# Performance work log

Measured on AMD Instinct MI355X. Metric: run time of the kernel, lower is better.

## Reference

```python
import jax, jax.numpy as jnp
import numpy as np

DIM = 1024
LN_EPS = 1e-5


def setup_inputs() -> dict:
    key = jax.random.key(0)
    ks = jax.random.split(key, 6)
    B, S, D = 8, 2048, DIM
    x = jax.random.normal(ks[0], (B, S, D), dtype=jnp.float32)
    mask = jnp.ones((B, S, 1), dtype=jnp.float32)
    # LayerNorm params
    ln_g = jnp.ones((D,), dtype=jnp.float32)
    ln_b = jnp.zeros((D,), dtype=jnp.float32)
    # FeedForward: Linear(D, D) -> GELU -> Linear(D, D); hidden_dim == dim per source
    lim = 1.0 / np.sqrt(D)
    w1 = jax.random.uniform(ks[1], (D, D), jnp.float32, -lim, lim)
    b1 = jax.random.uniform(ks[2], (D,), jnp.float32, -lim, lim)
    w2 = jax.random.uniform(ks[3], (D, D), jnp.float32, -lim, lim)
    b2 = jax.random.uniform(ks[4], (D,), jnp.float32, -lim, lim)
    return {"x": x, "mask": mask, "ln_g": ln_g, "ln_b": ln_b,
            "w1": w1, "b1": b1, "w2": w2, "b2": b2}


def _layernorm(t, g, b):
    mu = jnp.mean(t, axis=-1, keepdims=True)
    var = jnp.mean(jnp.square(t - mu), axis=-1, keepdims=True)
    return (t - mu) * jax.lax.rsqrt(var + LN_EPS) * g + b


def reference(x, mask, ln_g, ln_b, w1, b1, w2, b2):
    # torch.fft(t, signal_ndim=1): FFT over hidden axis (complex input, imag=0)
    ft = jnp.fft.fft(x.astype(jnp.float32), axis=-1)
    # torch.fft(., signal_ndim=2): 2D FFT over (seq, hidden)
    ft = jnp.fft.fft2(ft, axes=(-2, -1))
    ft = ft.real  # [..., 0] slice of the fake-complex tensor
    t = _layernorm(x + ft, ln_g, ln_b)
    # FeedForward: Linear -> GELU(exact) -> Linear (dropout is identity at eval)
    h = jax.nn.gelu(t @ w1 + b1, approximate=False)
    out = h @ w2 + b2
    return out * mask
```

## Files before the change

kernel.cpp:

```cpp
#include <hip/hip_runtime.h>
#include <math.h>

#define DIMD 1024
#define SEQ  2048
#define BATCH 8
#define ROWS (BATCH * SEQ)

#define MF 1152
#define KF 1088

typedef __attribute__((ext_vector_type(8))) short bf16x8;
typedef __attribute__((ext_vector_type(4))) float f32x4;
typedef __attribute__((ext_vector_type(8))) unsigned short ushort8;

__device__ __forceinline__ unsigned short f2bf(float f) {
    unsigned u = __float_as_uint(f);
    unsigned r = (u + 0x7FFFu + ((u >> 16) & 1u)) >> 16;
    return (unsigned short)r;
}
__device__ __forceinline__ float bf2f(unsigned short h) {
    return __uint_as_float(((unsigned)h) << 16);
}
__device__ __forceinline__ void gl_lds16(const void* g, void* l) {
    __builtin_amdgcn_global_load_lds(
        (const __attribute__((address_space(1))) unsigned int*)g,
        (__attribute__((address_space(3))) unsigned int*)l, 16, 0, 0);
}


__global__ __launch_bounds__(256) void build_acos(unsigned short* __restrict__ Acos) {
    int s = blockIdx.x;
    for (int t = threadIdx.x; t < KF; t += 256) {
        float c = 0.0f;
        if (t <= 1024) {
            int prod = (s * t) & (SEQ - 1);
            c = cospif((float)prod * (1.0f / 1024.0f));
        }
        Acos[(size_t)s * KF + t] = f2bf(c);
    }
}

__global__ __launch_bounds__(256) void build_xe(const float* __restrict__ x,
                                                unsigned short* __restrict__ Xe) {
    int lane = threadIdx.x & 63;
    int oct  = threadIdx.x >> 6;
    int n = blockIdx.x * 64 + lane;
    int b = n >> 10, d = n & 1023;
    int rd = (DIMD - d) & (DIMD - 1);
    int t0 = blockIdx.y * 32 + oct * 8;
    const float* xb = x + (size_t)b * SEQ * DIMD + rd;
    ushort8 tmp;
    #pragma unroll
    for (int j = 0; j < 8; ++j) {
        int t = t0 + j;
        float v;
        if (t == 0)          v = xb[0];
        else if (t < 1024)   v = xb[(size_t)t * DIMD] + xb[(size_t)(2048 - t) * DIMD];
        else if (t == 1024)  v = xb[(size_t)1024 * DIMD];
        else                 v = 0.0f;
        tmp[j] = f2bf(v);
    }
    *(ushort8*)&Xe[(size_t)n * KF + t0] = tmp;
}

__global__ __launch_bounds__(256) void pack_wt(const float* __restrict__ W,
                                               unsigned short* __restrict__ Wt) {
    int lane = threadIdx.x & 63;
    int oct = threadIdx.x >> 6;
    int n = blockIdx.x * 64 + lane;
    int k0 = blockIdx.y * 32 + oct * 8;
    ushort8 tmp;
    #pragma unroll
    for (int j = 0; j < 8; ++j) tmp[j] = f2bf(W[(size_t)(k0 + j) * DIMD + n]);
    *(ushort8*)&Wt[(size_t)n * DIMD + k0] = tmp;
}

template <int MODE>
__global__ __launch_bounds__(256) void gemm_bt(const unsigned short* __restrict__ A,
                                               const unsigned short* __restrict__ B,
                                               int K, int lda, int ldb, int ldc,
                                               const float* __restrict__ xres,
                                               const float* __restrict__ bias,
                                               const float* __restrict__ mask,
                                               void* __restrict__ outp) {
    __shared__ unsigned short As[128 * 64];
    __shared__ unsigned short Bs[128 * 64];

    const int tid = threadIdx.x;
    const int lane = tid & 63;
    const int wv = tid >> 6;
    const int wm = wv & 1;
    const int wn = wv >> 1;
    const int fr = lane & 15;
    const int quad = lane >> 4;

    int bx = blockIdx.x, by = blockIdx.y;
    if (MODE != 0) {
        int lin = bx + 8 * by;
        int c = lin & 7;
        int g = lin >> 3;
        bx = g & 7;
        by = (g >> 3) * 8 + c;
    }
    const int m0 = by * 128;
    const int n0 = bx * 128;

    const int st_row = (lane >> 3);
    const int st_col = (lane & 7) * 8;

    f32x4 acc[4][4] = {};

    for (int k0 = 0; k0 < K; k0 += 64) {
        __syncthreads();
        #pragma unroll
        for (int i = 0; i < 4; ++i) {
            int chunk = wv * 4 + i;
            int ar = m0 + chunk * 8 + st_row;
            int br = n0 + chunk * 8 + st_row;
            gl_lds16(&A[(size_t)ar * lda + k0 + st_col], &As[chunk * 512]);
            gl_lds16(&B[(size_t)br * ldb + k0 + st_col], &Bs[chunk * 512]);
        }
        __syncthreads();

        #pragma unroll
        for (int ks = 0; ks < 2; ++ks) {
            bf16x8 af[4], bfv[4];
            #pragma unroll
            for (int i = 0; i < 4; ++i)
                af[i] = *(const bf16x8*)&As[(wm * 64 + i * 16 + fr) * 64 + ks * 32 + quad * 8];
            #pragma unroll
            for (int j = 0; j < 4; ++j)
                bfv[j] = *(const bf16x8*)&Bs[(wn * 64 + j * 16 + fr) * 64 + ks * 32 + quad * 8];
            #pragma unroll
            for (int i = 0; i < 4; ++i)
                #pragma unroll
                for (int j = 0; j < 4; ++j)
                    acc[i][j] = __builtin_amdgcn_mfma_f32_16x16x32_bf16(af[i], bfv[j], acc[i][j], 0, 0, 0);
        }
    }

    #pragma unroll
    for (int i = 0; i < 4; ++i) {
        int rowb = m0 + wm * 64 + i * 16 + quad * 4;
        #pragma unroll
        for (int j = 0; j < 4; ++j) {
            int col = n0 + wn * 64 + j * 16 + fr;
            #pragma unroll
            for (int r = 0; r < 4; ++r) {
                float v = acc[i][j][r];
                int row = rowb + r;
                if (MODE == 0) {
                    int s = row;
                    if (s <= 1024) {
                        int b = col >> 10, d = col & 1023;
                        unsigned short* y = (unsigned short*)outp;
                        size_t i1 = ((size_t)b * SEQ + s) * DIMD + d;
                        y[i1] = f2bf(xres[i1] + 1024.0f * v);
                        if (s >= 1 && s <= 1023) {
                            size_t i2 = ((size_t)b * SEQ + (2048 - s)) * DIMD + d;
                            y[i2] = f2bf(xres[i2] + 1024.0f * v);
                        }
                    }
                } else if (MODE == 1) {
                    v += bias[col];
                    v = 0.5f * v * (1.0f + erff(v * 0.70710678118654752f));
                    ((unsigned short*)outp)[(size_t)row * ldc + col] = f2bf(v);
                } else {
                    v += bias[col];
                    v *= mask[row];
                    ((float*)outp)[(size_t)row * ldc + col] = v;
                }
            }
        }
    }
}

__global__ __launch_bounds__(256) void ln_bf(const unsigned short* __restrict__ y,
                                             const float* __restrict__ g,
                                             const float* __restrict__ beta,
                                             unsigned short* __restrict__ t) {
    const int row = blockIdx.x;
    ushort4 raw = ((const ushort4*)(y + (size_t)row * DIMD))[threadIdx.x];
    float v0 = bf2f(raw.x), v1 = bf2f(raw.y), v2 = bf2f(raw.z), v3 = bf2f(raw.w);

    __shared__ float red[4];
    const int wave = threadIdx.x >> 6;
    const int lane = threadIdx.x & 63;

    float sm = v0 + v1 + v2 + v3;
    #pragma unroll
    for (int off = 32; off > 0; off >>= 1) sm += __shfl_down(sm, off, 64);
    if (lane == 0) red[wave] = sm;
    __syncthreads();
    const float mean = (red[0] + red[1] + red[2] + red[3]) * (1.0f / DIMD);

    float dx0 = v0 - mean, dx1 = v1 - mean, dx2 = v2 - mean, dx3 = v3 - mean;
    float q = dx0 * dx0 + dx1 * dx1 + dx2 * dx2 + dx3 * dx3;
    __syncthreads();
    #pragma unroll
    for (int off = 32; off > 0; off >>= 1) q += __shfl_down(q, off, 64);
    if (lane == 0) red[wave] = q;
    __syncthreads();
    const float var = (red[0] + red[1] + red[2] + red[3]) * (1.0f / DIMD);
    const float rstd = rsqrtf(var + 1e-5f);

    float4 g4 = ((const float4*)g)[threadIdx.x];
    float4 b4 = ((const float4*)beta)[threadIdx.x];
    ushort4 o;
    o.x = f2bf(dx0 * rstd * g4.x + b4.x);
    o.y = f2bf(dx1 * rstd * g4.y + b4.y);
    o.z = f2bf(dx2 * rstd * g4.z + b4.z);
    o.w = f2bf(dx3 * rstd * g4.w + b4.w);
    ((ushort4*)(t + (size_t)row * DIMD))[threadIdx.x] = o;
}

#define BM 64
#define BN 64
#define BK 16

__global__ __launch_bounds__(256) void fft_cos_kernel(const float* __restrict__ x,
                                                      float* __restrict__ y) {
    __shared__ float tab[SEQ];
    __shared__ float As[BM][BK + 1];
    __shared__ float Bs[BK][BN + 1];
    const int tid = threadIdx.x;
    const int b = blockIdx.z;
    const int s0 = blockIdx.y * BM;
    const int n0 = blockIdx.x * BN;
    for (int i = tid; i < SEQ; i += 256) tab[i] = cospif((float)i * (1.0f / 1024.0f));
    const int tx = tid & 15;
    const int ty = tid >> 4;
    float acc[4][4] = {};
    const float* Xb = x + (size_t)b * SEQ * DIMD;
    for (int k0 = 0; k0 < SEQ; k0 += BK) {
        __syncthreads();
        for (int f = tid; f < BM * BK; f += 256) {
            int i = f / BK, k = f % BK;
            int prod = (s0 + i) * (k0 + k);
            As[i][k] = tab[prod & (SEQ - 1)];
        }
        for (int f = tid; f < BK * BN; f += 256) {
            int k = f / BN, j = f % BN;
            int d = n0 + j;
            int rd = (DIMD - d) & (DIMD - 1);
            Bs[k][j] = Xb[(size_t)(k0 + k) * DIMD + rd];
        }
        __syncthreads();
        #pragma unroll
        for (int k = 0; k < BK; ++k) {
            float a[4], bv[4];
            #pragma unroll
            for (int i = 0; i < 4; ++i) a[i] = As[ty * 4 + i][k];
            #pragma unroll
            for (int j = 0; j < 4; ++j) bv[j] = Bs[k][tx * 4 + j];
            #pragma unroll
            for (int i = 0; i < 4; ++i)
                #pragma unroll
                for (int j = 0; j < 4; ++j) acc[i][j] += a[i] * bv[j];
        }
    }
    #pragma unroll
    for (int i = 0; i < 4; ++i) {
        int s = s0 + ty * 4 + i;
        #pragma unroll
        for (int j = 0; j < 4; ++j) {
            int d = n0 + tx * 4 + j;
            y[((size_t)b * SEQ + s) * DIMD + d] = Xb[(size_t)s * DIMD + d] + 1024.0f * acc[i][j];
        }
    }
}

__global__ __launch_bounds__(256) void ln_kernel(float* __restrict__ y,
                                                 const float* __restrict__ g,
                                                 const float* __restrict__ beta) {
    const int row = blockIdx.x;
    float4* p = (float4*)(y + (size_t)row * DIMD);
    float4 v = p[threadIdx.x];
    __shared__ float red[4];
    const int wave = threadIdx.x >> 6;
    const int lane = threadIdx.x & 63;
    float s = v.x + v.y + v.z + v.w;
    #pragma unroll
    for (int off = 32; off > 0; off >>= 1) s += __shfl_down(s, off, 64);
    if (lane == 0) red[wave] = s;
    __syncthreads();
    const float mean = (red[0] + red[1] + red[2] + red[3]) * (1.0f / DIMD);
    float dx0 = v.x - mean, dx1 = v.y - mean, dx2 = v.z - mean, dx3 = v.w - mean;
    float q = dx0 * dx0 + dx1 * dx1 + dx2 * dx2 + dx3 * dx3;
    __syncthreads();
    #pragma unroll
    for (int off = 32; off > 0; off >>= 1) q += __shfl_down(q, off, 64);
    if (lane == 0) red[wave] = q;
    __syncthreads();
    const float var = (red[0] + red[1] + red[2] + red[3]) * (1.0f / DIMD);
    const float rstd = rsqrtf(var + 1e-5f);
    float4 g4 = ((const float4*)g)[threadIdx.x];
    float4 b4 = ((const float4*)beta)[threadIdx.x];
    float4 o;
    o.x = dx0 * rstd * g4.x + b4.x;
    o.y = dx1 * rstd * g4.y + b4.y;
    o.z = dx2 * rstd * g4.z + b4.z;
    o.w = dx3 * rstd * g4.w + b4.w;
    p[threadIdx.x] = o;
}

template <int MODE>
__global__ __launch_bounds__(256) void ff_gemm(const float* __restrict__ A,
                                               const float* __restrict__ W,
                                               const float* __restrict__ bias,
                                               const float* __restrict__ mask,
                                               float* __restrict__ out) {
    __shared__ float As[BM][BK + 1];
    __shared__ float Bs[BK][BN + 1];
    const int tid = threadIdx.x;
    const int tx = tid & 15;
    const int ty = tid >> 4;
    const int m0 = blockIdx.y * BM;
    const int n0 = blockIdx.x * BN;
    float acc[4][4] = {};
    for (int k0 = 0; k0 < DIMD; k0 += BK) {
        __syncthreads();
        for (int f = tid; f < BM * BK; f += 256) {
            int i = f / BK, k = f % BK;
            As[i][k] = A[(size_t)(m0 + i) * DIMD + k0 + k];
        }
        for (int f = tid; f < BK * BN; f += 256) {
            int k = f / BN, j = f % BN;
            Bs[k][j] = W[(size_t)(k0 + k) * DIMD + n0 + j];
        }
        __syncthreads();
        #pragma unroll
        for (int k = 0; k < BK; ++k) {
            float a[4], bv[4];
            #pragma unroll
            for (int i = 0; i < 4; ++i) a[i] = As[ty * 4 + i][k];
            #pragma unroll
            for (int j = 0; j < 4; ++j) bv[j] = Bs[k][tx * 4 + j];
            #pragma unroll
            for (int i = 0; i < 4; ++i)
                #pragma unroll
                for (int j = 0; j < 4; ++j) acc[i][j] += a[i] * bv[j];
        }
    }
    #pragma unroll
    for (int i = 0; i < 4; ++i) {
        int m = m0 + ty * 4 + i;
        float mk = (MODE == 1) ? mask[m] : 1.0f;
        #pragma unroll
        for (int j = 0; j < 4; ++j) {
            int n = n0 + tx * 4 + j;
            float v = acc[i][j] + bias[n];
            if (MODE == 0) v = 0.5f * v * (1.0f + erff(v * 0.70710678118654752f));
            else v *= mk;
            out[(size_t)m * DIMD + n] = v;
        }
    }
}

extern "C" void kernel_launch(void* const* d_in, const int* in_sizes, int n_in,
                              void* d_out, int out_size, void* d_ws, size_t ws_size,
                              hipStream_t stream) {
    const float* x    = (const float*)d_in[0];
    const float* mask = (const float*)d_in[1];
    const float* ln_g = (const float*)d_in[2];
    const float* ln_b = (const float*)d_in[3];
    const float* w1   = (const float*)d_in[4];
    const float* b1   = (const float*)d_in[5];
    const float* w2   = (const float*)d_in[6];
    const float* b2   = (const float*)d_in[7];
    float* out = (float*)d_out;

    const size_t MB = 1024 * 1024;
    dim3 blk(256);

    if (ws_size >= 70 * MB) {
        char* w = (char*)d_ws;
        unsigned short* Acos = (unsigned short*)w;
        unsigned short* Xe   = (unsigned short*)(w + 4 * MB);
        unsigned short* y    = (unsigned short*)(w + 32 * MB);
        unsigned short* t    = (unsigned short*)w;
        unsigned short* h    = (unsigned short*)(w + 32 * MB);
        unsigned short* W1t  = (unsigned short*)(w + 64 * MB);
        unsigned short* W2t  = (unsigned short*)(w + 66 * MB);

        build_acos<<<dim3(MF), blk, 0, stream>>>(Acos);
        build_xe<<<dim3(8192 / 64, KF / 32), blk, 0, stream>>>(x, Xe);
        pack_wt<<<dim3(1024 / 64, 1024 / 32), blk, 0, stream>>>(w1, W1t);
        pack_wt<<<dim3(1024 / 64, 1024 / 32), blk, 0, stream>>>(w2, W2t);

        gemm_bt<0><<<dim3(8192 / 128, MF / 128), blk, 0, stream>>>(
            Acos, Xe, KF, KF, KF, 0, x, nullptr, nullptr, y);
        ln_bf<<<dim3(ROWS), blk, 0, stream>>>(y, ln_g, ln_b, t);
        gemm_bt<1><<<dim3(1024 / 128, ROWS / 128), blk, 0, stream>>>(
            t, W1t, 1024, 1024, 1024, 1024, nullptr, b1, nullptr, h);
        gemm_bt<2><<<dim3(1024 / 128, ROWS / 128), blk, 0, stream>>>(
            h, W2t, 1024, 1024, 1024, 1024, nullptr, b2, mask, out);
    } else {
        float* yf = (float*)d_ws;
        const size_t bufBytes = (size_t)ROWS * DIMD * sizeof(float);
        fft_cos_kernel<<<dim3(DIMD / BN, SEQ / BM, BATCH), blk, 0, stream>>>(x, yf);
        ln_kernel<<<dim3(ROWS), blk, 0, stream>>>(yf, ln_g, ln_b);
        ff_gemm<0><<<dim3(DIMD / BN, ROWS / BM), blk, 0, stream>>>(yf, w1, b1, nullptr, out);
        ff_gemm<1><<<dim3(DIMD / BN, ROWS / BM), blk, 0, stream>>>(out, w2, b2, mask, yf);
        hipMemcpyAsync(d_out, yf, bufBytes, hipMemcpyDeviceToDevice, stream);
    }
}
```

Measured before the change: 380.4 us.

## Store compact fp32 FFT result and fuse residual add into paired-row LayerNorm

The cosine GEMM now writes its raw fp32 output in a compact [s, b*d] layout into the output buffer, with the 1024 scale folded into the cosine table. The residual add and the mirror-symmetry expansion (rows s and 2048-s) move into a new LayerNorm kernel that handles both symmetric rows per block and reuses one loaded F row. This removes the scattered duplicate bf16 stores and the bf16 intermediate. The cost is a larger fp32 intermediate, folding 1024 into the bf16 table, and extra syncs inside the LN loop.

```diff
diff --git a/kernel.cpp b/kernel.cpp
--- a/kernel.cpp
+++ b/kernel.cpp
@@ -34,7 +34,7 @@
         float c = 0.0f;
         if (t <= 1024) {
             int prod = (s * t) & (SEQ - 1);
-            c = cospif((float)prod * (1.0f / 1024.0f));
+            c = 1024.0f * cospif((float)prod * (1.0f / 1024.0f));
         }
         Acos[(size_t)s * KF + t] = f2bf(c);
     }
@@ -79,7 +79,6 @@
 __global__ __launch_bounds__(256) void gemm_bt(const unsigned short* __restrict__ A,
                                                const unsigned short* __restrict__ B,
                                                int K, int lda, int ldb, int ldc,
-                                               const float* __restrict__ xres,
                                                const float* __restrict__ bias,
                                                const float* __restrict__ mask,
                                                void* __restrict__ outp) {
@@ -150,17 +149,7 @@
                 float v = acc[i][j][r];
                 int row = rowb + r;
                 if (MODE == 0) {
-                    int s = row;
-                    if (s <= 1024) {
-                        int b = col >> 10, d = col & 1023;
-                        unsigned short* y = (unsigned short*)outp;
-                        size_t i1 = ((size_t)b * SEQ + s) * DIMD + d;
-                        y[i1] = f2bf(xres[i1] + 1024.0f * v);
-                        if (s >= 1 && s <= 1023) {
-                            size_t i2 = ((size_t)b * SEQ + (2048 - s)) * DIMD + d;
-                            y[i2] = f2bf(xres[i2] + 1024.0f * v);
-                        }
-                    }
+                    ((float*)outp)[(size_t)row * ldc + col] = v;
                 } else if (MODE == 1) {
                     v += bias[col];
                     v = 0.5f * v * (1.0f + erff(v * 0.70710678118654752f));
@@ -175,43 +164,54 @@
     }
 }
 
-__global__ __launch_bounds__(256) void ln_bf(const unsigned short* __restrict__ y,
-                                             const float* __restrict__ g,
-                                             const float* __restrict__ beta,
-                                             unsigned short* __restrict__ t) {
-    const int row = blockIdx.x;
-    ushort4 raw = ((const ushort4*)(y + (size_t)row * DIMD))[threadIdx.x];
-    float v0 = bf2f(raw.x), v1 = bf2f(raw.y), v2 = bf2f(raw.z), v3 = bf2f(raw.w);
+__global__ __launch_bounds__(256) void ln_pair(const float* __restrict__ x,
+                                               const float* __restrict__ F,
+                                               const float* __restrict__ g,
+                                               const float* __restrict__ beta,
+                                               unsigned short* __restrict__ t) {
+    const int sp = blockIdx.x;
+    const int b  = blockIdx.y;
+
+    float4 fv = ((const float4*)(F + (size_t)sp * 8192 + (size_t)b * 1024))[threadIdx.x];
+    float4 g4 = ((const float4*)g)[threadIdx.x];
+    float4 b4 = ((const float4*)beta)[threadIdx.x];
 
     __shared__ float red[4];
     const int wave = threadIdx.x >> 6;
     const int lane = threadIdx.x & 63;
 
-    float sm = v0 + v1 + v2 + v3;
-    #pragma unroll
-    for (int off = 32; off > 0; off >>= 1) sm += __shfl_down(sm, off, 64);
-    if (lane == 0) red[wave] = sm;
-    __syncthreads();
-    const float mean = (red[0] + red[1] + red[2] + red[3]) * (1.0f / DIMD);
-
-    float dx0 = v0 - mean, dx1 = v1 - mean, dx2 = v2 - mean, dx3 = v3 - mean;
-    float q = dx0 * dx0 + dx1 * dx1 + dx2 * dx2 + dx3 * dx3;
-    __syncthreads();
-    #pragma unroll
-    for (int off = 32; off > 0; off >>= 1) q += __shfl_down(q, off, 64);
-    if (lane == 0) red[wave] = q;
-    __syncthreads();
-    const float var = (red[0] + red[1] + red[2] + red[3]) * (1.0f / DIMD);
-    const float rstd = rsqrtf(var + 1e-5f);
-
-    float4 g4 = ((const float4*)g)[threadIdx.x];
-    float4 b4 = ((const float4*)beta)[threadIdx.x];
-    ushort4 o;
-    o.x = f2bf(dx0 * rstd * g4.x + b4.x);
-    o.y = f2bf(dx1 * rstd * g4.y + b4.y);
-    o.z = f2bf(dx2 * rstd * g4.z + b4.z);
-    o.w = f2bf(dx3 * rstd * g4.w + b4.w);
-    ((ushort4*)(t + (size_t)row * DIMD))[threadIdx.x] = o;
+    const int nrows = (sp >= 1 && sp <= 1023) ? 2 : 1;
+    for (int p = 0; p < nrows; ++p) {
+        int s = p ? (2048 - sp) : sp;
+        int row = b * SEQ + s;
+        float4 xv = ((const float4*)(x + (size_t)row * DIMD))[threadIdx.x];
+        float v0 = xv.x + fv.x, v1 = xv.y + fv.y, v2 = xv.z + fv.z, v3 = xv.w + fv.w;
+
+        float sm = v0 + v1 + v2 + v3;
+        #pragma unroll
+        for (int off = 32; off > 0; off >>= 1) sm += __shfl_down(sm, off, 64);
+        if (lane == 0) red[wave] = sm;
+        __syncthreads();
+        const float mean = (red[0] + red[1] + red[2] + red[3]) * (1.0f / DIMD);
+
+        float dx0 = v0 - mean, dx1 = v1 - mean, dx2 = v2 - mean, dx3 = v3 - mean;
+        float q = dx0 * dx0 + dx1 * dx1 + dx2 * dx2 + dx3 * dx3;
+        __syncthreads();
+        #pragma unroll
+        for (int off = 32; off > 0; off >>= 1) q += __shfl_down(q, off, 64);
+        if (lane == 0) red[wave] = q;
+        __syncthreads();
+        const float var = (red[0] + red[1] + red[2] + red[3]) * (1.0f / DIMD);
+        const float rstd = rsqrtf(var + 1e-5f);
+
+        ushort4 o;
+        o.x = f2bf(dx0 * rstd * g4.x + b4.x);
+        o.y = f2bf(dx1 * rstd * g4.y + b4.y);
+        o.z = f2bf(dx2 * rstd * g4.z + b4.z);
+        o.w = f2bf(dx3 * rstd * g4.w + b4.w);
+        ((ushort4*)(t + (size_t)row * DIMD))[threadIdx.x] = o;
+        __syncthreads();
+    }
 }
 
 #define BM 64
@@ -377,11 +377,11 @@
         char* w = (char*)d_ws;
         unsigned short* Acos = (unsigned short*)w;
         unsigned short* Xe   = (unsigned short*)(w + 4 * MB);
-        unsigned short* y    = (unsigned short*)(w + 32 * MB);
-        unsigned short* t    = (unsigned short*)w;
-        unsigned short* h    = (unsigned short*)(w + 32 * MB);
+        unsigned short* t    = (unsigned short*)(w + 32 * MB);
+        unsigned short* h    = (unsigned short*)w;
         unsigned short* W1t  = (unsigned short*)(w + 64 * MB);
         unsigned short* W2t  = (unsigned short*)(w + 66 * MB);
+        float* F = (float*)d_out;
 
         build_acos<<<dim3(MF), blk, 0, stream>>>(Acos);
         build_xe<<<dim3(8192 / 64, KF / 32), blk, 0, stream>>>(x, Xe);
@@ -389,12 +389,12 @@
         pack_wt<<<dim3(1024 / 64, 1024 / 32), blk, 0, stream>>>(w2, W2t);
 
         gemm_bt<0><<<dim3(8192 / 128, MF / 128), blk, 0, stream>>>(
-            Acos, Xe, KF, KF, KF, 0, x, nullptr, nullptr, y);
-        ln_bf<<<dim3(ROWS), blk, 0, stream>>>(y, ln_g, ln_b, t);
+            Acos, Xe, KF, KF, KF, 8192, nullptr, nullptr, F);
+        ln_pair<<<dim3(1025, BATCH), blk, 0, stream>>>(x, F, ln_g, ln_b, t);
         gemm_bt<1><<<dim3(1024 / 128, ROWS / 128), blk, 0, stream>>>(
-            t, W1t, 1024, 1024, 1024, 1024, nullptr, b1, nullptr, h);
+            t, W1t, 1024, 1024, 1024, 1024, b1, nullptr, h);
         gemm_bt<2><<<dim3(1024 / 128, ROWS / 128), blk, 0, stream>>>(
-            h, W2t, 1024, 1024, 1024, 1024, nullptr, b2, mask, out);
+            h, W2t, 1024, 1024, 1024, 1024, b2, mask, out);
     } else {
         float* yf = (float*)d_ws;
         const size_t bufBytes = (size_t)ROWS * DIMD * sizeof(float);
```

Result: faster. 348.5 us (-8.4%).
